# Optimization experiments

Hardware: AMD Instinct MI355X
Metric: run time of the kernel (lower is better)

Reference implementation:

```python
import jax, jax.numpy as jnp
import numpy as np
from jax import lax

HW = 256

def setup_inputs() -> dict:
    key = jax.random.key(0)
    k1, k2, k3 = jax.random.split(key, 3)
    B, C = 8, 64
    x1 = jax.random.normal(k1, (B, C, HW, HW), dtype=jnp.float32)
    x2 = jax.random.normal(k2, (B, C, HW, HW), dtype=jnp.float32)
    w = jnp.ones((1, 1, 3, 3), dtype=jnp.float32) / 9.0  # fixed box filter
    b = jax.random.normal(k3, (1,), dtype=jnp.float32) * 0.1  # conv bias
    return {"x1": x1, "x2": x2, "w": w, "b": b}

def _box_conv(y, w, b):
    # y: [B,1,H,W] ; 3x3 conv, stride 1, pad 1, plus bias
    out = lax.conv_general_dilated(
        y, w, window_strides=(1, 1), padding=[(1, 1), (1, 1)],
        dimension_numbers=("NCHW", "OIHW", "NCHW"))
    return out + b.reshape(1, -1, 1, 1)

def reference(x1, x2, w, b):
    # channel-wise L1 norm -> [B,1,H,W]
    n1 = jnp.sum(jnp.abs(x1), axis=-3).reshape(-1, 1, HW, HW)
    n2 = jnp.sum(jnp.abs(x2), axis=-3).reshape(-1, 1, HW, HW)
    c1 = _box_conv(n1, w, b)
    c2 = _box_conv(n2, w, b)
    denom = c1 + c2
    return x1 * c1 / denom + x2 * c2 / denom
```

## Files before the change

kernel.cpp:

```cpp
#include <hip/hip_runtime.h>

#define HWD 256
#define HW2 (HWD * HWD)
#define NB 8
#define NC 64
#define PLANE4 (HW2 / 4)

__global__ void norms_kernel(const float* __restrict__ x1,
                             const float* __restrict__ x2,
                             float* __restrict__ n1,
                             float* __restrict__ n2) {
    int t = blockIdx.x * blockDim.x + threadIdx.x;
    int b = t >> 14;
    int p = t & (PLANE4 - 1);

    const float4* x1v = (const float4*)(x1 + (size_t)b * NC * HW2) + p;
    const float4* x2v = (const float4*)(x2 + (size_t)b * NC * HW2) + p;

    float4 a1 = make_float4(0.f, 0.f, 0.f, 0.f);
    float4 a2 = make_float4(0.f, 0.f, 0.f, 0.f);

#pragma unroll 8
    for (int c = 0; c < NC; ++c) {
        float4 v1 = x1v[(size_t)c * PLANE4];
        float4 v2 = x2v[(size_t)c * PLANE4];
        a1.x += fabsf(v1.x); a1.y += fabsf(v1.y);
        a1.z += fabsf(v1.z); a1.w += fabsf(v1.w);
        a2.x += fabsf(v2.x); a2.y += fabsf(v2.y);
        a2.z += fabsf(v2.z); a2.w += fabsf(v2.w);
    }

    ((float4*)n1)[t] = a1;
    ((float4*)n2)[t] = a2;
}

__global__ void conv_ratio_kernel(const float* __restrict__ n1,
                                  const float* __restrict__ n2,
                                  const float* __restrict__ w,
                                  const float* __restrict__ bias,
                                  float* __restrict__ r) {
    int t = blockIdx.x * blockDim.x + threadIdx.x;
    int b = t >> 16;
    int sp = t & (HW2 - 1);
    int y = sp >> 8;
    int x = sp & (HWD - 1);

    const float* p1 = n1 + (size_t)b * HW2;
    const float* p2 = n2 + (size_t)b * HW2;

    float s1 = 0.f, s2 = 0.f;
#pragma unroll
    for (int dy = -1; dy <= 1; ++dy) {
        int yy = y + dy;
        if (yy < 0 || yy >= HWD) continue;
#pragma unroll
        for (int dx = -1; dx <= 1; ++dx) {
            int xx = x + dx;
            if (xx < 0 || xx >= HWD) continue;
            float wv = w[(dy + 1) * 3 + (dx + 1)];
            int o = yy * HWD + xx;
            s1 += wv * p1[o];
            s2 += wv * p2[o];
        }
    }
    float bv = bias[0];
    float c1 = s1 + bv;
    float c2 = s2 + bv;
    r[t] = c1 / (c1 + c2);
}

__global__ void blend_kernel(const float* __restrict__ x1,
                             const float* __restrict__ x2,
                             const float* __restrict__ r,
                             float* __restrict__ out) {
    size_t t = (size_t)blockIdx.x * blockDim.x + threadIdx.x;
    int sp4 = (int)(t & (PLANE4 - 1));
    int plane = (int)(t >> 14);
    int b = plane >> 6;

    float4 v1 = ((const float4*)x1)[t];
    float4 v2 = ((const float4*)x2)[t];
    float4 rv = ((const float4*)r)[(size_t)b * PLANE4 + sp4];

    float4 o;
    o.x = v1.x * rv.x + v2.x * (1.f - rv.x);
    o.y = v1.y * rv.y + v2.y * (1.f - rv.y);
    o.z = v1.z * rv.z + v2.z * (1.f - rv.z);
    o.w = v1.w * rv.w + v2.w * (1.f - rv.w);

    ((float4*)out)[t] = o;
}

extern "C" void kernel_launch(void* const* d_in, const int* in_sizes, int n_in,
                              void* d_out, int out_size, void* d_ws, size_t ws_size,
                              hipStream_t stream) {
    const float* x1 = (const float*)d_in[0];
    const float* x2 = (const float*)d_in[1];
    const float* w  = (const float*)d_in[2];
    const float* bv = (const float*)d_in[3];
    float* out = (float*)d_out;

    float* n1 = (float*)d_ws;
    float* n2 = n1 + (size_t)NB * HW2;
    float* r  = n2 + (size_t)NB * HW2;

    const int block = 256;

    norms_kernel<<<NB * PLANE4 / block, block, 0, stream>>>(x1, x2, n1, n2);
    conv_ratio_kernel<<<NB * HW2 / block, block, 0, stream>>>(n1, n2, w, bv, r);
    blend_kernel<<<(size_t)NB * NC * PLANE4 / block, block, 0, stream>>>(x1, x2, r, out);
}
```

Baseline: 379.9 us.

## Split channel reduction across wavefronts and batch channels per thread in blend

The norms kernel now splits the 64-channel reduction into four 16-channel slices handled by separate wavefronts, combining partials through shared memory. This quadruples the block count to raise memory-level parallelism. The blend kernel processes 8 channels per thread, reusing the loaded ratio and using nontemporal stores for the output. The cost is an extra barrier and shared-memory reduction, and fewer threads in blend.

```diff
diff --git a/kernel.cpp b/kernel.cpp
--- a/kernel.cpp
+++ b/kernel.cpp
@@ -6,22 +6,27 @@
 #define NC 64
 #define PLANE4 (HW2 / 4)
 
+typedef float floatx4 __attribute__((ext_vector_type(4)));
+
 __global__ void norms_kernel(const float* __restrict__ x1,
                              const float* __restrict__ x2,
                              float* __restrict__ n1,
                              float* __restrict__ n2) {
-    int t = blockIdx.x * blockDim.x + threadIdx.x;
-    int b = t >> 14;
-    int p = t & (PLANE4 - 1);
+    const int s = threadIdx.x & 63;
+    const int g = threadIdx.x >> 6;
+    const int blk = blockIdx.x;
+    const int b = blk >> 8;
+    const int p = ((blk & 255) << 6) + s;
 
-    const float4* x1v = (const float4*)(x1 + (size_t)b * NC * HW2) + p;
-    const float4* x2v = (const float4*)(x2 + (size_t)b * NC * HW2) + p;
+    const size_t base = (size_t)b * NC * PLANE4 + (size_t)g * 16 * PLANE4 + p;
+    const float4* x1v = (const float4*)x1 + base;
+    const float4* x2v = (const float4*)x2 + base;
 
     float4 a1 = make_float4(0.f, 0.f, 0.f, 0.f);
     float4 a2 = make_float4(0.f, 0.f, 0.f, 0.f);
 
-#pragma unroll 8
-    for (int c = 0; c < NC; ++c) {
+#pragma unroll
+    for (int c = 0; c < 16; ++c) {
         float4 v1 = x1v[(size_t)c * PLANE4];
         float4 v2 = x2v[(size_t)c * PLANE4];
         a1.x += fabsf(v1.x); a1.y += fabsf(v1.y);
@@ -30,8 +35,30 @@
         a2.z += fabsf(v2.z); a2.w += fabsf(v2.w);
     }
 
-    ((float4*)n1)[t] = a1;
-    ((float4*)n2)[t] = a2;
+    __shared__ float4 l1[4][64];
+    __shared__ float4 l2[4][64];
+    l1[g][s] = a1;
+    l2[g][s] = a2;
+    __syncthreads();
+
+    const size_t oidx = (size_t)b * PLANE4 + p;
+    if (g == 0) {
+        float4 r0 = l1[0][s], r1 = l1[1][s], r2 = l1[2][s], r3 = l1[3][s];
+        float4 o;
+        o.x = (r0.x + r1.x) + (r2.x + r3.x);
+        o.y = (r0.y + r1.y) + (r2.y + r3.y);
+        o.z = (r0.z + r1.z) + (r2.z + r3.z);
+        o.w = (r0.w + r1.w) + (r2.w + r3.w);
+        ((float4*)n1)[oidx] = o;
+    } else if (g == 1) {
+        float4 r0 = l2[0][s], r1 = l2[1][s], r2 = l2[2][s], r3 = l2[3][s];
+        float4 o;
+        o.x = (r0.x + r1.x) + (r2.x + r3.x);
+        o.y = (r0.y + r1.y) + (r2.y + r3.y);
+        o.z = (r0.z + r1.z) + (r2.z + r3.z);
+        o.w = (r0.w + r1.w) + (r2.w + r3.w);
+        ((float4*)n2)[oidx] = o;
+    }
 }
 
 __global__ void conv_ratio_kernel(const float* __restrict__ n1,
@@ -73,22 +100,32 @@
                              const float* __restrict__ x2,
                              const float* __restrict__ r,
                              float* __restrict__ out) {
-    size_t t = (size_t)blockIdx.x * blockDim.x + threadIdx.x;
-    int sp4 = (int)(t & (PLANE4 - 1));
-    int plane = (int)(t >> 14);
-    int b = plane >> 6;
+    int t = blockIdx.x * blockDim.x + threadIdx.x;
+    int p = t & (PLANE4 - 1);
+    int cg = (t >> 14) & 7;
+    int b = t >> 17;
 
-    float4 v1 = ((const float4*)x1)[t];
-    float4 v2 = ((const float4*)x2)[t];
-    float4 rv = ((const float4*)r)[(size_t)b * PLANE4 + sp4];
+    float4 rv = ((const float4*)r)[(size_t)b * PLANE4 + p];
+    float4 one_m;
+    one_m.x = 1.f - rv.x; one_m.y = 1.f - rv.y;
+    one_m.z = 1.f - rv.z; one_m.w = 1.f - rv.w;
 
-    float4 o;
-    o.x = v1.x * rv.x + v2.x * (1.f - rv.x);
-    o.y = v1.y * rv.y + v2.y * (1.f - rv.y);
-    o.z = v1.z * rv.z + v2.z * (1.f - rv.z);
-    o.w = v1.w * rv.w + v2.w * (1.f - rv.w);
+    size_t base = ((size_t)b * NC + (size_t)cg * 8) * PLANE4 + p;
+    const float4* x1v = (const float4*)x1 + base;
+    const float4* x2v = (const float4*)x2 + base;
+    floatx4* ov = (floatx4*)out + base;
 
-    ((float4*)out)[t] = o;
+#pragma unroll
+    for (int c = 0; c < 8; ++c) {
+        float4 v1 = x1v[(size_t)c * PLANE4];
+        float4 v2 = x2v[(size_t)c * PLANE4];
+        floatx4 o;
+        o.x = v1.x * rv.x + v2.x * one_m.x;
+        o.y = v1.y * rv.y + v2.y * one_m.y;
+        o.z = v1.z * rv.z + v2.z * one_m.z;
+        o.w = v1.w * rv.w + v2.w * one_m.w;
+        __builtin_nontemporal_store(o, ov + (size_t)c * PLANE4);
+    }
 }
 
 extern "C" void kernel_launch(void* const* d_in, const int* in_sizes, int n_in,
@@ -106,7 +143,7 @@
 
     const int block = 256;
 
-    norms_kernel<<<NB * PLANE4 / block, block, 0, stream>>>(x1, x2, n1, n2);
+    norms_kernel<<<NB * (PLANE4 / 64), block, 0, stream>>>(x1, x2, n1, n2);
     conv_ratio_kernel<<<NB * HW2 / block, block, 0, stream>>>(n1, n2, w, bv, r);
-    blend_kernel<<<(size_t)NB * NC * PLANE4 / block, block, 0, stream>>>(x1, x2, r, out);
+    blend_kernel<<<NB * (NC / 8) * PLANE4 / block, block, 0, stream>>>(x1, x2, r, out);
 }
```

New measurement: 360.9 us. 5.0% less time.
